# Kernel optimization log

Hardware: AMD Instinct MI355X
Metric: run time of the kernel (lower is better)

Reference implementation:

```python
import jax, jax.numpy as jnp
import numpy as np

B, C, H, W = 2, 1, 2048, 2048
RADIUS = 1
RK = 2 * RADIUS + 1  # 3
N = H * W
OBV_DECAY = 0.95


def setup_inputs() -> dict:
    key = jax.random.key(0)
    k1, k2, k3, k4, k5 = jax.random.split(key, 5)
    # x: [B, C+1, H, W]; channel 0 = spin field s, last channel = inverse temperature b (>0)
    x = jax.random.uniform(k1, (B, C + 1, H, W), dtype=jnp.float32)
    obvs = jax.random.uniform(k2, (B, 4, H, W), dtype=jnp.float32)
    # learned coupling table, center tap zeroed (no self-coupling)
    J = jax.random.uniform(k3, (1, RK * RK, N), dtype=jnp.float32)
    J = J.at[:, RADIUS * RK + RADIUS, :].set(0.0)
    # explicit RNG draws (torch.rand_like equivalents) for determinism
    rand_s = jax.random.uniform(k4, (B, C, H, W), dtype=jnp.float32)
    rand_drop = jax.random.uniform(k5, (1, 1, H, W), dtype=jnp.float32)
    return {"x": x, "obvs": obvs, "J": J, "rand_s": rand_s, "rand_drop": rand_drop}


def _unfold3(s):
    # F.unfold(circular_pad(s,1), 3) for a single-channel map: [B,1,H,W] -> [B,9,H*W]
    sp = jnp.pad(s, ((0, 0), (0, 0), (1, 1), (1, 1)), mode='wrap')
    patches = jnp.stack(
        [sp[:, 0, i:i + H, j:j + W] for i in range(RK) for j in range(RK)], axis=1
    )  # [B, 9, H, W], kernel positions row-major (matches F.unfold)
    return patches.reshape(s.shape[0], RK * RK, N)


def reference(x, obvs, J, rand_s, rand_drop):
    s = x[:, :C]          # [B,1,H,W] spins
    b = x[:, -1:]         # [B,1,H,W] inverse temperature
    sf = s.reshape(s.shape[0], 1, N)                 # unfold(s, 1)
    sJs = 2.0 * sf * (_unfold3(s) * J)               # [B,9,N]
    delta_e = sJs.sum(axis=1).reshape(s.shape)       # [B,1,H,W]
    E = -0.5 * delta_e

    # EMA observables
    e, e2, c, m = obvs[:, 0:1], obvs[:, 1:2], obvs[:, 2:3], obvs[:, 3:4]
    d = OBV_DECAY
    e = d * e + (1.0 - d) * E
    e2 = d * e2 + (1.0 - d) * E ** 2
    c = d * c + (1.0 - d) * (e2 - e ** 2) * b ** 2
    m = d * m + (1.0 - d) * s
    obvs_out = jnp.concatenate([e, e2, c, m], axis=1)  # [B,4,H,W]

    p = jnp.where(delta_e <= 0.0, jnp.ones_like(s), jnp.exp(-delta_e * b))
    accept = (rand_s < p) & (rand_drop > 0.5)
    flip = -2.0 * accept.astype(s.dtype) + 1.0

    state = jnp.concatenate([s * flip, b], axis=1)    # [B,2,H,W]
    return state, obvs_out
```

## Files before the change

### kernel.cpp

```cpp
#include <hip/hip_runtime.h>
#include <math.h>

namespace {
constexpr int H = 2048;
constexpr int W = 2048;
constexpr int NPIX = H * W;
constexpr int B = 2;
constexpr float DECf = 0.95f;
constexpr float OMDf = 1.0f - 0.95f;
}

using f4 = __attribute__((ext_vector_type(4))) float;

__global__ __launch_bounds__(256, 4) void ising_step_kernel(
    const float* __restrict__ x,
    const float* __restrict__ obvs,
    const float* __restrict__ Jm,
    const float* __restrict__ rs,
    const float* __restrict__ rd,
    float* __restrict__ out)
{
  __shared__ float lr[3][520];

  const int bid = blockIdx.x;
  const int u   = ((bid & 7) << 10) | (bid >> 3);
  const int bi  = u & 1;
  const int pu  = u >> 1;
  const int h   = pu >> 1;
  const int t   = threadIdx.x;
  const int w0b = (pu & 1) << 10;
  const int w0  = w0b | (t << 2);
  const int n0  = (h << 11) | w0;

  const float* sbase = x + (size_t)bi * 2 * NPIX;
  const int hm = (h - 1) & (H - 1);
  const int hp = (h + 1) & (H - 1);
  const float* rowm = sbase + (size_t)hm * W;
  const float* rowc = sbase + (size_t)h  * W;
  const float* rowp = sbase + (size_t)hp * W;

  const f4 vm = *(const f4*)(rowm + w0);
  const f4 vc = *(const f4*)(rowc + w0);
  const f4 vp = *(const f4*)(rowp + w0);

  f4 jv[8];
  #pragma unroll
  for (int k = 0; k < 8; ++k) {
    const int kk = (k < 4) ? k : (k + 1);
    jv[k] = *(const f4*)(Jm + (size_t)kk * NPIX + n0);
  }
  const f4 bv  = *(const f4*)(sbase + (size_t)NPIX + n0);
  const float* ob = obvs + (size_t)bi * 4 * NPIX + n0;
  const f4 ev  = *(const f4*)(ob);
  const f4 e2v = *(const f4*)(ob + (size_t)NPIX);
  const f4 cv  = *(const f4*)(ob + 2 * (size_t)NPIX);
  const f4 mv  = *(const f4*)(ob + 3 * (size_t)NPIX);
  const f4 rv  = *(const f4*)(rs + (size_t)bi * NPIX + n0);
  const f4 dv  = *(const f4*)(rd + n0);

  lr[0][2 * t] = vm.x;  lr[0][2 * t + 3] = vm.w;
  lr[1][2 * t] = vc.x;  lr[1][2 * t + 3] = vc.w;
  lr[2][2 * t] = vp.x;  lr[2][2 * t + 3] = vp.w;
  if (t < 6) {
    const int r    = t >> 1;
    const int side = t & 1;
    const float* rowr = (r == 0) ? rowm : ((r == 1) ? rowc : rowp);
    const int wsrc = side ? ((w0b + 1024) & (W - 1)) : ((w0b - 1) & (W - 1));
    lr[r][side ? 512 : 1] = rowr[wsrc];
  }
  __syncthreads();
  const float Lm = lr[0][2 * t + 1], Rm = lr[0][2 * t + 2];
  const float Lc = lr[1][2 * t + 1], Rc = lr[1][2 * t + 2];
  const float Lp = lr[2][2 * t + 1], Rp = lr[2][2 * t + 2];

  const float am[6] = {Lm, vm.x, vm.y, vm.z, vm.w, Rm};
  const float ac[6] = {Lc, vc.x, vc.y, vc.z, vc.w, Rc};
  const float ap[6] = {Lp, vp.x, vp.y, vp.z, vp.w, Rp};

  const float bq[4]  = {bv.x, bv.y, bv.z, bv.w};
  const float eq[4]  = {ev.x, ev.y, ev.z, ev.w};
  const float e2q[4] = {e2v.x, e2v.y, e2v.z, e2v.w};
  const float cq[4]  = {cv.x, cv.y, cv.z, cv.w};
  const float mq[4]  = {mv.x, mv.y, mv.z, mv.w};
  const float rsq[4] = {rv.x, rv.y, rv.z, rv.w};
  const float rdq[4] = {dv.x, dv.y, dv.z, dv.w};

  float so[4], eo[4], e2o[4], co[4], mo[4];
  #pragma unroll
  for (int tt = 0; tt < 4; ++tt) {
    const double sum =
        (double)jv[0][tt] * am[tt]     + (double)jv[1][tt] * am[tt + 1] +
        (double)jv[2][tt] * am[tt + 2] + (double)jv[3][tt] * ac[tt]     +
        (double)jv[4][tt] * ac[tt + 2] + (double)jv[5][tt] * ap[tt]     +
        (double)jv[6][tt] * ap[tt + 1] + (double)jv[7][tt] * ap[tt + 2];
    const float sf  = ac[tt + 1];
    const double s  = (double)sf;
    const double de = 2.0 * s * sum;
    const double p  = (de <= 0.0) ? 1.0 : exp(-de * (double)bq[tt]);
    const bool acc  = ((double)rsq[tt] < p) && (rdq[tt] > 0.5f);
    const float E   = (float)(-s * sum);
    const float bf  = bq[tt];
    const float en  = DECf * eq[tt]  + OMDf * E;
    const float e2n = DECf * e2q[tt] + OMDf * E * E;
    const float cn  = DECf * cq[tt]  + OMDf * (e2n - en * en) * bf * bf;
    const float mn  = DECf * mq[tt]  + OMDf * sf;
    so[tt]  = acc ? -sf : sf;
    eo[tt]  = en;
    e2o[tt] = e2n;
    co[tt]  = cn;
    mo[tt]  = mn;
  }

  float* st = out + (size_t)bi * 2 * NPIX;
  float* oo = out + (size_t)B * 2 * NPIX + (size_t)bi * 4 * NPIX;
  __builtin_nontemporal_store((f4){so[0], so[1], so[2], so[3]}, (f4*)(st + n0));
  __builtin_nontemporal_store(bv, (f4*)(st + (size_t)NPIX + n0));
  __builtin_nontemporal_store((f4){eo[0], eo[1], eo[2], eo[3]}, (f4*)(oo + n0));
  __builtin_nontemporal_store((f4){e2o[0], e2o[1], e2o[2], e2o[3]},
                              (f4*)(oo + (size_t)NPIX + n0));
  __builtin_nontemporal_store((f4){co[0], co[1], co[2], co[3]},
                              (f4*)(oo + 2 * (size_t)NPIX + n0));
  __builtin_nontemporal_store((f4){mo[0], mo[1], mo[2], mo[3]},
                              (f4*)(oo + 3 * (size_t)NPIX + n0));
}

extern "C" void kernel_launch(void* const* d_in, const int* in_sizes, int n_in,
                              void* d_out, int out_size, void* d_ws, size_t ws_size,
                              hipStream_t stream) {
  const float* x    = (const float*)d_in[0];
  const float* obvs = (const float*)d_in[1];
  const float* Jm   = (const float*)d_in[2];
  const float* rs   = (const float*)d_in[3];
  const float* rd   = (const float*)d_in[4];
  float* out = (float*)d_out;

  constexpr int grid = B * H * 2;
  ising_step_kernel<<<grid, 256, 0, stream>>>(x, obvs, Jm, rs, rd, out);
}
```

Measured before the change: 110.1 us.

## Process both batch elements per block to share J and dropout loads

```diff
diff --git a/kernel.cpp b/kernel.cpp
--- a/kernel.cpp
+++ b/kernel.cpp
@@ -12,7 +12,7 @@
 
 using f4 = __attribute__((ext_vector_type(4))) float;
 
-__global__ __launch_bounds__(256, 4) void ising_step_kernel(
+__global__ __launch_bounds__(256) void ising_step_kernel(
     const float* __restrict__ x,
     const float* __restrict__ obvs,
     const float* __restrict__ Jm,
@@ -20,28 +20,34 @@
     const float* __restrict__ rd,
     float* __restrict__ out)
 {
-  __shared__ float lr[3][520];
+  __shared__ float lr[2][3][520];
 
   const int bid = blockIdx.x;
-  const int u   = ((bid & 7) << 10) | (bid >> 3);
-  const int bi  = u & 1;
-  const int pu  = u >> 1;
-  const int h   = pu >> 1;
+  const int u   = ((bid & 7) << 9) | (bid >> 3);
+  const int h   = u >> 1;
   const int t   = threadIdx.x;
-  const int w0b = (pu & 1) << 10;
+  const int w0b = (u & 1) << 10;
   const int w0  = w0b | (t << 2);
   const int n0  = (h << 11) | w0;
 
-  const float* sbase = x + (size_t)bi * 2 * NPIX;
   const int hm = (h - 1) & (H - 1);
   const int hp = (h + 1) & (H - 1);
-  const float* rowm = sbase + (size_t)hm * W;
-  const float* rowc = sbase + (size_t)h  * W;
-  const float* rowp = sbase + (size_t)hp * W;
 
-  const f4 vm = *(const f4*)(rowm + w0);
-  const f4 vc = *(const f4*)(rowc + w0);
-  const f4 vp = *(const f4*)(rowp + w0);
+  const float* rowp_[2][3];
+  #pragma unroll
+  for (int bi = 0; bi < 2; ++bi) {
+    const float* sb = x + (size_t)bi * 2 * NPIX;
+    rowp_[bi][0] = sb + (size_t)hm * W;
+    rowp_[bi][1] = sb + (size_t)h  * W;
+    rowp_[bi][2] = sb + (size_t)hp * W;
+  }
+
+  f4 vrow[2][3];
+  #pragma unroll
+  for (int bi = 0; bi < 2; ++bi)
+    #pragma unroll
+    for (int r = 0; r < 3; ++r)
+      vrow[bi][r] = *(const f4*)(rowp_[bi][r] + w0);
 
   f4 jv[8];
   #pragma unroll
@@ -49,79 +55,94 @@
     const int kk = (k < 4) ? k : (k + 1);
     jv[k] = *(const f4*)(Jm + (size_t)kk * NPIX + n0);
   }
-  const f4 bv  = *(const f4*)(sbase + (size_t)NPIX + n0);
-  const float* ob = obvs + (size_t)bi * 4 * NPIX + n0;
-  const f4 ev  = *(const f4*)(ob);
-  const f4 e2v = *(const f4*)(ob + (size_t)NPIX);
-  const f4 cv  = *(const f4*)(ob + 2 * (size_t)NPIX);
-  const f4 mv  = *(const f4*)(ob + 3 * (size_t)NPIX);
-  const f4 rv  = *(const f4*)(rs + (size_t)bi * NPIX + n0);
-  const f4 dv  = *(const f4*)(rd + n0);
+  const f4 dv = *(const f4*)(rd + n0);
 
-  lr[0][2 * t] = vm.x;  lr[0][2 * t + 3] = vm.w;
-  lr[1][2 * t] = vc.x;  lr[1][2 * t + 3] = vc.w;
-  lr[2][2 * t] = vp.x;  lr[2][2 * t + 3] = vp.w;
-  if (t < 6) {
-    const int r    = t >> 1;
-    const int side = t & 1;
-    const float* rowr = (r == 0) ? rowm : ((r == 1) ? rowc : rowp);
+  f4 bv[2], ev[2], e2v[2], cv[2], mv[2], rv[2];
+  #pragma unroll
+  for (int bi = 0; bi < 2; ++bi) {
+    const float* sb = x + (size_t)bi * 2 * NPIX;
+    bv[bi] = *(const f4*)(sb + (size_t)NPIX + n0);
+    const float* ob = obvs + (size_t)bi * 4 * NPIX + n0;
+    ev[bi]  = *(const f4*)(ob);
+    e2v[bi] = *(const f4*)(ob + (size_t)NPIX);
+    cv[bi]  = *(const f4*)(ob + 2 * (size_t)NPIX);
+    mv[bi]  = *(const f4*)(ob + 3 * (size_t)NPIX);
+    rv[bi]  = *(const f4*)(rs + (size_t)bi * NPIX + n0);
+  }
+
+  #pragma unroll
+  for (int bi = 0; bi < 2; ++bi)
+    #pragma unroll
+    for (int r = 0; r < 3; ++r) {
+      lr[bi][r][2 * t]     = vrow[bi][r].x;
+      lr[bi][r][2 * t + 3] = vrow[bi][r].w;
+    }
+  if (t < 12) {
+    const int bsel = t / 6;
+    const int rem  = t % 6;
+    const int r    = rem >> 1;
+    const int side = rem & 1;
+    const float* rp = rowp_[bsel][r];
     const int wsrc = side ? ((w0b + 1024) & (W - 1)) : ((w0b - 1) & (W - 1));
-    lr[r][side ? 512 : 1] = rowr[wsrc];
+    lr[bsel][r][side ? 512 : 1] = rp[wsrc];
   }
   __syncthreads();
-  const float Lm = lr[0][2 * t + 1], Rm = lr[0][2 * t + 2];
-  const float Lc = lr[1][2 * t + 1], Rc = lr[1][2 * t + 2];
-  const float Lp = lr[2][2 * t + 1], Rp = lr[2][2 * t + 2];
 
-  const float am[6] = {Lm, vm.x, vm.y, vm.z, vm.w, Rm};
-  const float ac[6] = {Lc, vc.x, vc.y, vc.z, vc.w, Rc};
-  const float ap[6] = {Lp, vp.x, vp.y, vp.z, vp.w, Rp};
+  #pragma unroll
+  for (int bi = 0; bi < 2; ++bi) {
+    const float Lm = lr[bi][0][2 * t + 1], Rm = lr[bi][0][2 * t + 2];
+    const float Lc = lr[bi][1][2 * t + 1], Rc = lr[bi][1][2 * t + 2];
+    const float Lp = lr[bi][2][2 * t + 1], Rp = lr[bi][2][2 * t + 2];
+    const f4 vm = vrow[bi][0], vc = vrow[bi][1], vp = vrow[bi][2];
+    const float am[6] = {Lm, vm.x, vm.y, vm.z, vm.w, Rm};
+    const float ac[6] = {Lc, vc.x, vc.y, vc.z, vc.w, Rc};
+    const float ap[6] = {Lp, vp.x, vp.y, vp.z, vp.w, Rp};
+    const float bq[4]  = {bv[bi].x, bv[bi].y, bv[bi].z, bv[bi].w};
+    const float eq[4]  = {ev[bi].x, ev[bi].y, ev[bi].z, ev[bi].w};
+    const float e2q[4] = {e2v[bi].x, e2v[bi].y, e2v[bi].z, e2v[bi].w};
+    const float cq[4]  = {cv[bi].x, cv[bi].y, cv[bi].z, cv[bi].w};
+    const float mq[4]  = {mv[bi].x, mv[bi].y, mv[bi].z, mv[bi].w};
+    const float rsq[4] = {rv[bi].x, rv[bi].y, rv[bi].z, rv[bi].w};
+    const float rdq[4] = {dv.x, dv.y, dv.z, dv.w};
 
-  const float bq[4]  = {bv.x, bv.y, bv.z, bv.w};
-  const float eq[4]  = {ev.x, ev.y, ev.z, ev.w};
-  const float e2q[4] = {e2v.x, e2v.y, e2v.z, e2v.w};
-  const float cq[4]  = {cv.x, cv.y, cv.z, cv.w};
-  const float mq[4]  = {mv.x, mv.y, mv.z, mv.w};
-  const float rsq[4] = {rv.x, rv.y, rv.z, rv.w};
-  const float rdq[4] = {dv.x, dv.y, dv.z, dv.w};
+    float so[4], eo[4], e2o[4], co[4], mo[4];
+    #pragma unroll
+    for (int tt = 0; tt < 4; ++tt) {
+      const double sum =
+          (double)jv[0][tt] * am[tt]     + (double)jv[1][tt] * am[tt + 1] +
+          (double)jv[2][tt] * am[tt + 2] + (double)jv[3][tt] * ac[tt]     +
+          (double)jv[4][tt] * ac[tt + 2] + (double)jv[5][tt] * ap[tt]     +
+          (double)jv[6][tt] * ap[tt + 1] + (double)jv[7][tt] * ap[tt + 2];
+      const float sf  = ac[tt + 1];
+      const double s  = (double)sf;
+      const double de = 2.0 * s * sum;
+      const double p  = (de <= 0.0) ? 1.0 : exp(-de * (double)bq[tt]);
+      const bool acc  = ((double)rsq[tt] < p) && (rdq[tt] > 0.5f);
+      const float E   = (float)(-s * sum);
+      const float bf  = bq[tt];
+      const float en  = DECf * eq[tt]  + OMDf * E;
+      const float e2n = DECf * e2q[tt] + OMDf * E * E;
+      const float cn  = DECf * cq[tt]  + OMDf * (e2n - en * en) * bf * bf;
+      const float mn  = DECf * mq[tt]  + OMDf * sf;
+      so[tt]  = acc ? -sf : sf;
+      eo[tt]  = en;
+      e2o[tt] = e2n;
+      co[tt]  = cn;
+      mo[tt]  = mn;
+    }
 
-  float so[4], eo[4], e2o[4], co[4], mo[4];
-  #pragma unroll
-  for (int tt = 0; tt < 4; ++tt) {
-    const double sum =
-        (double)jv[0][tt] * am[tt]     + (double)jv[1][tt] * am[tt + 1] +
-        (double)jv[2][tt] * am[tt + 2] + (double)jv[3][tt] * ac[tt]     +
-        (double)jv[4][tt] * ac[tt + 2] + (double)jv[5][tt] * ap[tt]     +
-        (double)jv[6][tt] * ap[tt + 1] + (double)jv[7][tt] * ap[tt + 2];
-    const float sf  = ac[tt + 1];
-    const double s  = (double)sf;
-    const double de = 2.0 * s * sum;
-    const double p  = (de <= 0.0) ? 1.0 : exp(-de * (double)bq[tt]);
-    const bool acc  = ((double)rsq[tt] < p) && (rdq[tt] > 0.5f);
-    const float E   = (float)(-s * sum);
-    const float bf  = bq[tt];
-    const float en  = DECf * eq[tt]  + OMDf * E;
-    const float e2n = DECf * e2q[tt] + OMDf * E * E;
-    const float cn  = DECf * cq[tt]  + OMDf * (e2n - en * en) * bf * bf;
-    const float mn  = DECf * mq[tt]  + OMDf * sf;
-    so[tt]  = acc ? -sf : sf;
-    eo[tt]  = en;
-    e2o[tt] = e2n;
-    co[tt]  = cn;
-    mo[tt]  = mn;
+    float* st = out + (size_t)bi * 2 * NPIX;
+    float* oo = out + (size_t)B * 2 * NPIX + (size_t)bi * 4 * NPIX;
+    __builtin_nontemporal_store((f4){so[0], so[1], so[2], so[3]}, (f4*)(st + n0));
+    __builtin_nontemporal_store(bv[bi], (f4*)(st + (size_t)NPIX + n0));
+    __builtin_nontemporal_store((f4){eo[0], eo[1], eo[2], eo[3]}, (f4*)(oo + n0));
+    __builtin_nontemporal_store((f4){e2o[0], e2o[1], e2o[2], e2o[3]},
+                                (f4*)(oo + (size_t)NPIX + n0));
+    __builtin_nontemporal_store((f4){co[0], co[1], co[2], co[3]},
+                                (f4*)(oo + 2 * (size_t)NPIX + n0));
+    __builtin_nontemporal_store((f4){mo[0], mo[1], mo[2], mo[3]},
+                                (f4*)(oo + 3 * (size_t)NPIX + n0));
   }
-
-  float* st = out + (size_t)bi * 2 * NPIX;
-  float* oo = out + (size_t)B * 2 * NPIX + (size_t)bi * 4 * NPIX;
-  __builtin_nontemporal_store((f4){so[0], so[1], so[2], so[3]}, (f4*)(st + n0));
-  __builtin_nontemporal_store(bv, (f4*)(st + (size_t)NPIX + n0));
-  __builtin_nontemporal_store((f4){eo[0], eo[1], eo[2], eo[3]}, (f4*)(oo + n0));
-  __builtin_nontemporal_store((f4){e2o[0], e2o[1], e2o[2], e2o[3]},
-                              (f4*)(oo + (size_t)NPIX + n0));
-  __builtin_nontemporal_store((f4){co[0], co[1], co[2], co[3]},
-                              (f4*)(oo + 2 * (size_t)NPIX + n0));
-  __builtin_nontemporal_store((f4){mo[0], mo[1], mo[2], mo[3]},
-                              (f4*)(oo + 3 * (size_t)NPIX + n0));
 }
 
 extern "C" void kernel_launch(void* const* d_in, const int* in_sizes, int n_in,
@@ -134,6 +155,6 @@
   const float* rd   = (const float*)d_in[4];
   float* out = (float*)d_out;
 
-  constexpr int grid = B * H * 2;
+  constexpr int grid = H * 2;
   ising_step_kernel<<<grid, 256, 0, stream>>>(x, obvs, Jm, rs, rd, out);
 }
```

Measured after the change: 117.5 us. +6.7%, slower.
